# Kernel tuning notes

Hardware: AMD Instinct MI355X
Metric: run time of the kernel (lower is better)

## Reference

```python
import jax, jax.numpy as jnp
import numpy as np
import math

B, S, D = 2, 2048, 2048
H, KV = 16, 4
HD = D // H          # 128
REP = H // KV        # 4


def setup_inputs() -> dict:
    key = jax.random.key(0)
    ks = jax.random.split(key, 6)
    x = jax.random.normal(ks[0], (B, S, D), dtype=jnp.float32)
    wq = jax.random.normal(ks[1], (D, D), dtype=jnp.float32) * (D ** -0.5)
    wk = jax.random.normal(ks[2], (KV * HD, D), dtype=jnp.float32) * (D ** -0.5)
    wv = jax.random.normal(ks[3], (KV * HD, D), dtype=jnp.float32) * (D ** -0.5)
    wo = jax.random.normal(ks[4], (D, D), dtype=jnp.float32) * (D ** -0.5)
    # RoPE frequencies: theta_i = 10000^(-2i/hd), angle = pos * theta_i
    inv_freq = 1.0 / (10000.0 ** (np.arange(0, HD, 2, dtype=np.float32) / HD))
    angles = np.arange(S, dtype=np.float32)[:, None] * inv_freq[None, :]  # [S, HD/2]
    freqs_cos = jnp.asarray(np.cos(angles), dtype=jnp.float32)
    freqs_sin = jnp.asarray(np.sin(angles), dtype=jnp.float32)
    return {"x": x, "wq": wq, "wk": wk, "wv": wv, "wo": wo,
            "freqs_cos": freqs_cos, "freqs_sin": freqs_sin}


def _rope(t, cos, sin):
    # t: [B, S, h, HD]; cos/sin: [S, HD/2]; complex multiply on (even, odd) pairs
    tr = t.reshape(*t.shape[:-1], HD // 2, 2)
    t0, t1 = tr[..., 0], tr[..., 1]
    c = cos[None, :, None, :]
    s = sin[None, :, None, :]
    o0 = t0 * c - t1 * s
    o1 = t0 * s + t1 * c
    return jnp.stack([o0, o1], axis=-1).reshape(t.shape)


def reference(x, wq, wk, wv, wo, freqs_cos, freqs_sin):
    # projections (torch Linear: y = x @ W.T)
    q = jnp.einsum('bsd,ed->bse', x, wq).reshape(B, S, H, HD)
    k = jnp.einsum('bsd,ed->bse', x, wk).reshape(B, S, KV, HD)
    v = jnp.einsum('bsd,ed->bse', x, wv).reshape(B, S, KV, HD)
    q = _rope(q, freqs_cos, freqs_sin)
    k = _rope(k, freqs_cos, freqs_sin)
    # GQA: repeat each kv head REP times -> [B, S, H, HD]
    k = jnp.repeat(k, REP, axis=2)
    v = jnp.repeat(v, REP, axis=2)
    # [B, H, S, HD]
    q = q.transpose(0, 2, 1, 3)
    k = k.transpose(0, 2, 1, 3)
    v = v.transpose(0, 2, 1, 3)
    scores = jnp.einsum('bhqd,bhkd->bhqk', q, k) * (1.0 / math.sqrt(HD))
    # faithful to torch: tril then masked_fill(scores == 0, -inf)
    scores = jnp.tril(scores)
    scores = jnp.where(scores == 0.0, -jnp.inf, scores)
    attn = jax.nn.softmax(scores, axis=-1)
    out = jnp.einsum('bhqk,bhkd->bhqd', attn, v)
    out = out.transpose(0, 2, 1, 3).reshape(B, S, D)
    return jnp.einsum('bsd,ed->bse', out, wo)
```

## Files before the change

kernel.cpp:

```cpp
#include <hip/hip_runtime.h>
#include <stdint.h>

#define B_ 2
#define S_ 2048
#define D_ 2048
#define NH 16
#define NKV 4
#define HD_ 128

typedef unsigned short u16;
typedef unsigned int u32;
typedef __attribute__((ext_vector_type(8))) __bf16 bf16x8;
typedef __attribute__((ext_vector_type(4))) float f32x4;
typedef __attribute__((ext_vector_type(16))) float f32x16;
typedef __attribute__((ext_vector_type(4))) unsigned int u32x4;
typedef __attribute__((ext_vector_type(8))) unsigned short ushort8v;

__device__ __forceinline__ u16 f2bf(float f) {
  u32 u = __builtin_bit_cast(u32, f);
  u32 r = (u + 0x7FFFu + ((u >> 16) & 1u)) >> 16;
  return (u16)r;
}
__device__ __forceinline__ float bf2f(u16 h) {
  return __builtin_bit_cast(float, ((u32)h) << 16);
}
__device__ __forceinline__ u32 cvtpk(float lo, float hi) {
  u32 r;
  asm("v_cvt_pk_bf16_f32 %0, %1, %2" : "=v"(r) : "v"(lo), "v"(hi));
  return r;
}
__device__ __forceinline__ float fexp2(float x) {
  float r;
  asm("v_exp_f32 %0, %1" : "=v"(r) : "v"(x));
  return r;
}
__device__ __forceinline__ f32x16 zero16() {
  f32x16 v;
#pragma unroll
  for (int i = 0; i < 16; ++i) v[i] = 0.f;
  return v;
}

__device__ __forceinline__ void gld_lds16(const void* g, void* l) {
  __builtin_amdgcn_global_load_lds(
      (const __attribute__((address_space(1))) void*)g,
      (__attribute__((address_space(3))) void*)l, 16, 0, 0);
}

#define QSCALE 0.12750527540095196f

__device__ __forceinline__ void cv8(const float* s, u16* d, int i) {
  const float4* sp = (const float4*)s + 2 * (size_t)i;
  float4 a = sp[0], b = sp[1];
  ushort8v o;
  o[0] = f2bf(a.x); o[1] = f2bf(a.y); o[2] = f2bf(a.z); o[3] = f2bf(a.w);
  o[4] = f2bf(b.x); o[5] = f2bf(b.y); o[6] = f2bf(b.z); o[7] = f2bf(b.w);
  *((ushort8v*)d + i) = o;
}
__global__ __launch_bounds__(256) void k_f2b_all(const float* __restrict__ x,
    const float* __restrict__ wq, const float* __restrict__ wk,
    const float* __restrict__ wv, const float* __restrict__ wo,
    u16* __restrict__ xb, u16* __restrict__ wqkv, u16* __restrict__ wob) {
  int i = blockIdx.x * 256 + threadIdx.x;
  if (i < 1048576) { cv8(x, xb, i); return; }
  i -= 1048576;
  if (i < 524288) { cv8(wq, wqkv, i); return; }
  i -= 524288;
  if (i < 131072) { cv8(wk, wqkv + 2048 * 2048, i); return; }
  i -= 131072;
  if (i < 131072) { cv8(wv, wqkv + 2560 * 2048, i); return; }
  i -= 131072;
  if (i < 524288) cv8(wo, wob, i);
}

__global__ __launch_bounds__(256) void k_gemm_qkv(const u16* __restrict__ A,
    const u16* __restrict__ W, u16* __restrict__ Qd, u16* __restrict__ Kd,
    u16* __restrict__ Vd, const float* __restrict__ fc,
    const float* __restrict__ fs, int K) {
  __shared__ char lds[32768];
  char* ldsA = lds;
  char* ldsB = lds + 16384;
  const int tid = threadIdx.x;
  const int lane = tid & 63;
  const int wave = tid >> 6;
  const int m0 = blockIdx.x * 128, n0 = blockIdx.y * 128;
  const int wm = (wave >> 1) * 64, wn = (wave & 1) * 64;
  f32x4 acc[4][4];
#pragma unroll
  for (int i = 0; i < 4; ++i)
#pragma unroll
    for (int j = 0; j < 4; ++j) acc[i][j] = f32x4{0.f, 0.f, 0.f, 0.f};
  const size_t Kb2 = (size_t)K * 2;
  int rowS[4], colS[4];
#pragma unroll
  for (int j = 0; j < 4; ++j) {
    int plin = j * 4096 + tid * 16;
    int o = plin ^ (((plin >> 7) & 7) << 4);
    rowS[j] = o >> 7;
    colS[j] = o & 127;
  }
  for (int kt = 0; kt < K; kt += 64) {
#pragma unroll
    for (int j = 0; j < 4; ++j) {
      gld_lds16((const char*)A + (size_t)(m0 + rowS[j]) * Kb2 + (size_t)kt * 2 + colS[j],
                ldsA + j * 4096 + wave * 1024);
      gld_lds16((const char*)W + (size_t)(n0 + rowS[j]) * Kb2 + (size_t)kt * 2 + colS[j],
                ldsB + j * 4096 + wave * 1024);
    }
    __syncthreads();
#pragma unroll
    for (int kk = 0; kk < 2; ++kk) {
      const int colb = kk * 64 + ((lane >> 4) << 4);
      bf16x8 af[4], bfv[4];
#pragma unroll
      for (int mi = 0; mi < 4; ++mi) {
        int row = wm + mi * 16 + (lane & 15);
        af[mi] = *(const bf16x8*)(ldsA + (row << 7) + (colb ^ ((row & 7) << 4)));
      }
#pragma unroll
      for (int ni = 0; ni < 4; ++ni) {
        int row = wn + ni * 16 + (lane & 15);
        bfv[ni] = *(const bf16x8*)(ldsB + (row << 7) + (colb ^ ((row & 7) << 4)));
      }
#pragma unroll
      for (int mi = 0; mi < 4; ++mi)
#pragma unroll
        for (int ni = 0; ni < 4; ++ni)
          acc[mi][ni] = __builtin_amdgcn_mfma_f32_16x16x32_bf16(af[mi], bfv[ni], acc[mi][ni], 0, 0, 0);
    }
    __syncthreads();
  }
  const int seg = blockIdx.y;
  const int bb = m0 >> 11;
  if (seg < 20) {
    const bool isQ = (seg < 16);
    const int h = isQ ? seg : seg - 16;
    u16* dstB = isQ ? (Qd + ((size_t)(bb * NH + h)) * S_ * HD_)
                    : (Kd + ((size_t)(bb * NKV + h)) * S_ * HD_);
    const float sc = isQ ? QSCALE : 1.0f;
#pragma unroll
    for (int ni = 0; ni < 4; ++ni) {
      const int c = wn + ni * 16 + (lane & 15);
      const int j = c >> 1;
#pragma unroll
      for (int mi = 0; mi < 4; ++mi)
#pragma unroll
        for (int r = 0; r < 4; ++r) {
          const int m = m0 + wm + mi * 16 + ((lane >> 4) << 2) + r;
          const int s = m & 2047;
          float val = acc[mi][ni][r];
          float par = __shfl_xor(val, 1);
          float cs = fc[s * 64 + j], sn = fs[s * 64 + j];
          float outv = (c & 1) ? (par * sn + val * cs) : (val * cs - par * sn);
          dstB[(size_t)s * HD_ + c] = f2bf(outv * sc);
        }
    }
  } else {
    const int h = seg - 20;
    u16* dstB = Vd + ((size_t)(bb * NKV + h)) * S_ * HD_;
#pragma unroll
    for (int ni = 0; ni < 4; ++ni) {
      const int c = wn + ni * 16 + (lane & 15);
#pragma unroll
      for (int mi = 0; mi < 4; ++mi)
#pragma unroll
        for (int r = 0; r < 4; ++r) {
          const int m = m0 + wm + mi * 16 + ((lane >> 4) << 2) + r;
          const int s = m & 2047;
          dstB[(size_t)s * HD_ + c] = f2bf(acc[mi][ni][r]);
        }
    }
  }
}

__global__ __launch_bounds__(512, 1) void k_gemm_out(const u16* __restrict__ A,
    const u16* __restrict__ W, float* __restrict__ C, int N, int K) {
  __shared__ char lds[2][49152];
  const int tid = threadIdx.x, lane = tid & 63, wave = tid >> 6;
  const int wm = wave >> 2, wn = wave & 3;
  const int m0 = blockIdx.x * 256, n0 = blockIdx.y * 128;
  const size_t Kb2 = (size_t)K * 2;
  f32x4 acc[8][2];
#pragma unroll
  for (int mi = 0; mi < 8; ++mi)
#pragma unroll
    for (int ni = 0; ni < 2; ++ni) acc[mi][ni] = f32x4{0.f, 0.f, 0.f, 0.f};
  int rA[4], cA[4], rB[2], cB[2];
#pragma unroll
  for (int j = 0; j < 4; ++j) {
    int p = j * 8192 + tid * 16;
    int o = p ^ (((p >> 7) & 7) << 4);
    rA[j] = o >> 7; cA[j] = o & 127;
  }
#pragma unroll
  for (int j = 0; j < 2; ++j) {
    int p = j * 8192 + tid * 16;
    int o = p ^ (((p >> 7) & 7) << 4);
    rB[j] = o >> 7; cB[j] = o & 127;
  }
  auto stage = [&](int t) {
    char* dst = &lds[t & 1][0];
    const char* As = (const char*)A + (size_t)t * 128;
    const char* Ws = (const char*)W + (size_t)t * 128;
#pragma unroll
    for (int j = 0; j < 4; ++j)
      gld_lds16(As + (size_t)(m0 + rA[j]) * Kb2 + cA[j], dst + j * 8192 + tid * 16);
#pragma unroll
    for (int j = 0; j < 2; ++j)
      gld_lds16(Ws + (size_t)(n0 + rB[j]) * Kb2 + cB[j], dst + 32768 + j * 8192 + tid * 16);
  };
  stage(0);
  __syncthreads();
  const int nt = K >> 6;
  for (int t = 0; t < nt; ++t) {
    if (t + 1 < nt) stage(t + 1);
    const char* buf = &lds[t & 1][0];
#pragma unroll
    for (int kk = 0; kk < 2; ++kk) {
      const int cb = kk * 64 + ((lane >> 4) << 4);
      bf16x8 af[8], bfr[2];
#pragma unroll
      for (int mi = 0; mi < 8; ++mi) {
        int r = wm * 128 + mi * 16 + (lane & 15);
        af[mi] = *(const bf16x8*)(buf + (r << 7) + (cb ^ ((r & 7) << 4)));
      }
#pragma unroll
      for (int ni = 0; ni < 2; ++ni) {
        int r = wn * 32 + ni * 16 + (lane & 15);
        bfr[ni] = *(const bf16x8*)(buf + 32768 + (r << 7) + (cb ^ ((r & 7) << 4)));
      }
      __builtin_amdgcn_s_setprio(1);
#pragma unroll
      for (int mi = 0; mi < 8; ++mi)
#pragma unroll
        for (int ni = 0; ni < 2; ++ni)
          acc[mi][ni] = __builtin_amdgcn_mfma_f32_16x16x32_bf16(af[mi], bfr[ni], acc[mi][ni], 0, 0, 0);
      __builtin_amdgcn_s_setprio(0);
    }
    __syncthreads();
  }
#pragma unroll
  for (int mi = 0; mi < 8; ++mi)
#pragma unroll
    for (int ni = 0; ni < 2; ++ni) {
      const int n = n0 + wn * 32 + ni * 16 + (lane & 15);
#pragma unroll
      for (int r = 0; r < 4; ++r) {
        const int m = m0 + wm * 128 + mi * 16 + ((lane >> 4) << 2) + r;
        C[(size_t)m * N + n] = acc[mi][ni][r];
      }
    }
}

__global__ __launch_bounds__(256, 2) void k_attn(const u16* __restrict__ Q,
    const u16* __restrict__ Kt, const u16* __restrict__ Vt, u16* __restrict__ O) {
  __shared__ char kls[2][16384];
  __shared__ char vls[2][16384];
  const int h = blockIdx.x, b = blockIdx.y;
  const int z = blockIdx.z;
  const int qtb = (z < 8) ? (15 - z) : (z - 8);
  const int tid = threadIdx.x, lane = tid & 63, wave = tid >> 6;
  const int ql = lane & 31, g = lane >> 5;
  const int kvh = h >> 2;
  const u16* Qb = Q + ((size_t)(b * NH + h)) * S_ * HD_;
  const u16* Kb = Kt + ((size_t)(b * NKV + kvh)) * S_ * HD_;
  const u16* Vb = Vt + ((size_t)(b * NKV + kvh)) * S_ * HD_;
  const int q0 = qtb * 128, qw0 = q0 + wave * 32;
  const int qme = qw0 + ql;
  int kRowS[4], kColS[4];
#pragma unroll
  for (int j = 0; j < 4; ++j) {
    int plin = j * 4096 + tid * 16;
    int o = plin ^ (((plin >> 8) & 7) << 4);
    kRowS[j] = o >> 8;
    kColS[j] = o & 255;
  }
  const int kp = tid & 31, hb = (tid >> 5) * 16;
  auto loadV = [&](int tn, u32* vr0, u32* vr1) {
    const u16* vp = Vb + (size_t)(tn * 64 + 2 * kp) * HD_ + hb;
    const u32* r0 = (const u32*)vp;
    const u32* r1 = (const u32*)(vp + HD_);
#pragma unroll
    for (int wd = 0; wd < 8; ++wd) { vr0[wd] = r0[wd]; vr1[wd] = r1[wd]; }
  };
  auto writeV = [&](char* vn, const u32* vr0, const u32* vr1) {
#pragma unroll
    for (int wd = 0; wd < 8; ++wd) {
      u32 v0 = vr0[wd], v1 = vr1[wd];
      u32 lo = (v0 & 0xFFFFu) | (v1 << 16);
      u32 hi = (v0 >> 16) | (v1 & 0xFFFF0000u);
      int hd0 = hb + 2 * wd, hd1 = hd0 + 1;
      *(u32*)(vn + hd0 * 128 + ((4 * kp) ^ ((hd0 & 7) << 4))) = lo;
      *(u32*)(vn + hd1 * 128 + ((4 * kp) ^ ((hd1 & 7) << 4))) = hi;
    }
  };

#pragma unroll
  for (int j = 0; j < 4; ++j)
    gld_lds16((const char*)Kb + (size_t)kRowS[j] * 256 + kColS[j],
              &kls[0][0] + j * 4096 + wave * 1024);
  u32 pv0[8], pv1[8];
  loadV(0, pv0, pv1);
  bf16x8 qf[8];
#pragma unroll
  for (int kk = 0; kk < 8; ++kk)
    qf[kk] = *(const bf16x8*)(Qb + (size_t)qme * HD_ + kk * 16 + g * 8);
  writeV(&vls[0][0], pv0, pv1);
  __syncthreads();

  f32x16 oacc[4];
#pragma unroll
  for (int th = 0; th < 4; ++th) oacc[th] = zero16();
  float mrun = -1e30f, lrun = 0.0f;
  const int nt = 2 * qtb + 2;

  int cur = 0;
  for (int t = 0; t < nt; ++t) {
    const int kv0 = t * 64;
    const bool haveNext = (t + 1 < nt);
    u32 vr0[8], vr1[8];
    if (haveNext) {
      const int kvn = kv0 + 64;
#pragma unroll
      for (int j = 0; j < 4; ++j)
        gld_lds16((const char*)Kb + (size_t)(kvn + kRowS[j]) * 256 + kColS[j],
                  &kls[cur ^ 1][0] + j * 4096 + wave * 1024);
      loadV(t + 1, vr0, vr1);
    }
    if (kv0 <= qw0 + 31) {
      const char* kcur = &kls[cur][0];
      const char* vcur = &vls[cur][0];
      f32x16 c0 = zero16(), c1 = zero16();
      __builtin_amdgcn_s_setprio(1);
#pragma unroll
      for (int kk = 0; kk < 8; ++kk) {
        const int sw = (kk * 32 + 16 * g) ^ ((ql & 7) << 4);
        bf16x8 kf0 = *(const bf16x8*)(kcur + (ql << 8) + sw);
        bf16x8 kf1 = *(const bf16x8*)(kcur + ((32 + ql) << 8) + sw);
        c0 = __builtin_amdgcn_mfma_f32_32x32x16_bf16(kf0, qf[kk], c0, 0, 0, 0);
        c1 = __builtin_amdgcn_mfma_f32_32x32x16_bf16(kf1, qf[kk], c1, 0, 0, 0);
      }
      __builtin_amdgcn_s_setprio(0);
      const bool diag = (kv0 + 63 > qw0);
      float mt = -1e30f;
      if (diag) {
#pragma unroll
        for (int r = 0; r < 16; ++r) {
          float s0 = c0[r], s1 = c1[r];
          int kb = kv0 + (r & 3) + ((r >> 2) << 3) + 4 * g;
          if (kb > qme) s0 = -1e30f;
          if (kb + 32 > qme) s1 = -1e30f;
          c0[r] = s0; c1[r] = s1;
          mt = fmaxf(mt, fmaxf(s0, s1));
        }
      } else {
#pragma unroll
        for (int r = 0; r < 16; ++r)
          mt = fmaxf(mt, fmaxf(c0[r], c1[r]));
      }
      mt = fmaxf(mt, __shfl_xor(mt, 32));
      if (!__all(mt <= mrun + 8.0f)) {
        float mnew = fmaxf(mrun, mt);
        float alpha = fexp2(mrun - mnew);
        lrun *= alpha;
        mrun = mnew;
#pragma unroll
        for (int r = 0; r < 16; ++r) {
          float av = __shfl(alpha, 36 * g + (r & 3) + ((r >> 2) << 3));
          oacc[0][r] *= av; oacc[1][r] *= av;
          oacc[2][r] *= av; oacc[3][r] *= av;
        }
      }
      float lt = 0.0f;
#pragma unroll
      for (int r = 0; r < 16; ++r) {
        float p0 = fexp2(c0[r] - mrun);
        float p1 = fexp2(c1[r] - mrun);
        c0[r] = p0; c1[r] = p1;
        lt += p0 + p1;
      }
      lt += __shfl_xor(lt, 32);
      lrun += lt;
      u32 paw[4][4];
#pragma unroll
      for (int a = 0; a < 2; ++a) {
        {
          u32 X = cvtpk(c0[8 * a + 0], c0[8 * a + 1]);
          u32 Y = cvtpk(c0[8 * a + 2], c0[8 * a + 3]);
          u32 Z = cvtpk(c0[8 * a + 4], c0[8 * a + 5]);
          u32 W = cvtpk(c0[8 * a + 6], c0[8 * a + 7]);
          u32 S1 = g ? X : Z, S2 = g ? Y : W;
          u32 R1 = (u32)__shfl_xor((int)S1, 32), R2 = (u32)__shfl_xor((int)S2, 32);
          paw[a][0] = g ? R1 : X; paw[a][1] = g ? R2 : Y;
          paw[a][2] = g ? Z : R1; paw[a][3] = g ? W : R2;
        }
        {
          u32 X = cvtpk(c1[8 * a + 0], c1[8 * a + 1]);
          u32 Y = cvtpk(c1[8 * a + 2], c1[8 * a + 3]);
          u32 Z = cvtpk(c1[8 * a + 4], c1[8 * a + 5]);
          u32 W = cvtpk(c1[8 * a + 6], c1[8 * a + 7]);
          u32 S1 = g ? X : Z, S2 = g ? Y : W;
          u32 R1 = (u32)__shfl_xor((int)S1, 32), R2 = (u32)__shfl_xor((int)S2, 32);
          paw[2 + a][0] = g ? R1 : X; paw[2 + a][1] = g ? R2 : Y;
          paw[2 + a][2] = g ? Z : R1; paw[2 + a][3] = g ? W : R2;
        }
      }
      __builtin_amdgcn_s_setprio(1);
#pragma unroll
      for (int ks = 0; ks < 4; ++ks) {
        bf16x8 pf = __builtin_bit_cast(bf16x8,
            u32x4{paw[ks][0], paw[ks][1], paw[ks][2], paw[ks][3]});
        const int cb = (32 * ks + 16 * g) ^ ((ql & 7) << 4);
#pragma unroll
        for (int th = 0; th < 4; ++th) {
          bf16x8 vf = *(const bf16x8*)(vcur + ((th * 32 + ql) << 7) + cb);
          oacc[th] = __builtin_amdgcn_mfma_f32_32x32x16_bf16(pf, vf, oacc[th], 0, 0, 0);
        }
      }
      __builtin_amdgcn_s_setprio(0);
    }
    if (haveNext) writeV(&vls[cur ^ 1][0], vr0, vr1);
    __syncthreads();
    cur ^= 1;
  }
#pragma unroll
  for (int r = 0; r < 16; ++r) {
    float lr = __shfl(lrun, 36 * g + (r & 3) + ((r >> 2) << 3));
    float li = 1.0f / lr;
    int q = qw0 + (r & 3) + ((r >> 2) << 3) + 4 * g;
    size_t rowo = (size_t)(b * S_ + q) * D_ + h * HD_ + ql;
#pragma unroll
    for (int th = 0; th < 4; ++th)
      O[rowo + 32 * th] = f2bf(oacc[th][r] * li);
  }
}

extern "C" void kernel_launch(void* const* d_in, const int* in_sizes, int n_in,
                              void* d_out, int out_size, void* d_ws, size_t ws_size,
                              hipStream_t stream) {
  const float* x  = (const float*)d_in[0];
  const float* wq = (const float*)d_in[1];
  const float* wk = (const float*)d_in[2];
  const float* wv = (const float*)d_in[3];
  const float* wo = (const float*)d_in[4];
  const float* fc = (const float*)d_in[5];
  const float* fs = (const float*)d_in[6];
  float* out = (float*)d_out;
  char* ws = (char*)d_ws;
  const size_t MB = 1ull << 20;
  u16* xb   = (u16*)(ws);
  u16* wqkv = (u16*)(ws + 16 * MB);
  u16* wob  = (u16*)(ws + 28 * MB);
  u16* Qb   = (u16*)(ws + 36 * MB);
  u16* Kb   = (u16*)(ws + 52 * MB);
  u16* Vb   = (u16*)(ws + 56 * MB);
  u16* attb = (u16*)(ws);

  k_f2b_all<<<dim3(9216), dim3(256), 0, stream>>>(x, wq, wk, wv, wo, xb, wqkv, wob);

  k_gemm_qkv<<<dim3(32, 24), dim3(256), 0, stream>>>(xb, wqkv, Qb, Kb, Vb, fc, fs, D_);

  k_attn<<<dim3(NH, B_, 16), dim3(256), 0, stream>>>(Qb, Kb, Vb, attb);

  k_gemm_out<<<dim3(16, 16), dim3(512), 0, stream>>>(attb, wob, out, D_, D_);
}
```

Measured before the change: 218.1 us.

## Rewrite QKV GEMM with 256x128 tiles, 8 waves and double-buffered LDS

```diff
diff --git a/kernel.cpp b/kernel.cpp
--- a/kernel.cpp
+++ b/kernel.cpp
@@ -73,60 +73,71 @@
   if (i < 524288) cv8(wo, wob, i);
 }
 
-__global__ __launch_bounds__(256) void k_gemm_qkv(const u16* __restrict__ A,
+__global__ __launch_bounds__(512, 1) void k_gemm_qkv(const u16* __restrict__ A,
     const u16* __restrict__ W, u16* __restrict__ Qd, u16* __restrict__ Kd,
     u16* __restrict__ Vd, const float* __restrict__ fc,
     const float* __restrict__ fs, int K) {
-  __shared__ char lds[32768];
-  char* ldsA = lds;
-  char* ldsB = lds + 16384;
-  const int tid = threadIdx.x;
-  const int lane = tid & 63;
-  const int wave = tid >> 6;
-  const int m0 = blockIdx.x * 128, n0 = blockIdx.y * 128;
-  const int wm = (wave >> 1) * 64, wn = (wave & 1) * 64;
-  f32x4 acc[4][4];
-#pragma unroll
-  for (int i = 0; i < 4; ++i)
-#pragma unroll
-    for (int j = 0; j < 4; ++j) acc[i][j] = f32x4{0.f, 0.f, 0.f, 0.f};
+  __shared__ char lds[2][49152];
+  const int tid = threadIdx.x, lane = tid & 63, wave = tid >> 6;
+  const int wm = wave >> 2, wn = wave & 3;
+  const int m0 = blockIdx.x * 256, n0 = blockIdx.y * 128;
   const size_t Kb2 = (size_t)K * 2;
-  int rowS[4], colS[4];
+  f32x4 acc[8][2];
+#pragma unroll
+  for (int mi = 0; mi < 8; ++mi)
+#pragma unroll
+    for (int ni = 0; ni < 2; ++ni) acc[mi][ni] = f32x4{0.f, 0.f, 0.f, 0.f};
+  int rA[4], cA[4], rB[2], cB[2];
 #pragma unroll
   for (int j = 0; j < 4; ++j) {
-    int plin = j * 4096 + tid * 16;
-    int o = plin ^ (((plin >> 7) & 7) << 4);
-    rowS[j] = o >> 7;
-    colS[j] = o & 127;
-  }
-  for (int kt = 0; kt < K; kt += 64) {
-#pragma unroll
-    for (int j = 0; j < 4; ++j) {
-      gld_lds16((const char*)A + (size_t)(m0 + rowS[j]) * Kb2 + (size_t)kt * 2 + colS[j],
-                ldsA + j * 4096 + wave * 1024);
-      gld_lds16((const char*)W + (size_t)(n0 + rowS[j]) * Kb2 + (size_t)kt * 2 + colS[j],
-                ldsB + j * 4096 + wave * 1024);
-    }
-    __syncthreads();
+    int p = j * 8192 + tid * 16;
+    int o = p ^ (((p >> 7) & 7) << 4);
+    rA[j] = o >> 7; cA[j] = o & 127;
+  }
+#pragma unroll
+  for (int j = 0; j < 2; ++j) {
+    int p = j * 8192 + tid * 16;
+    int o = p ^ (((p >> 7) & 7) << 4);
+    rB[j] = o >> 7; cB[j] = o & 127;
+  }
+  auto stage = [&](int t) {
+    char* dst = &lds[t & 1][0];
+    const char* As = (const char*)A + (size_t)t * 128;
+    const char* Ws = (const char*)W + (size_t)t * 128;
+#pragma unroll
+    for (int j = 0; j < 4; ++j)
+      gld_lds16(As + (size_t)(m0 + rA[j]) * Kb2 + cA[j], dst + j * 8192 + tid * 16);
+#pragma unroll
+    for (int j = 0; j < 2; ++j)
+      gld_lds16(Ws + (size_t)(n0 + rB[j]) * Kb2 + cB[j], dst + 32768 + j * 8192 + tid * 16);
+  };
+  stage(0);
+  __syncthreads();
+  const int nt = K >> 6;
+  for (int t = 0; t < nt; ++t) {
+    if (t + 1 < nt) stage(t + 1);
+    const char* buf = &lds[t & 1][0];
 #pragma unroll
     for (int kk = 0; kk < 2; ++kk) {
-      const int colb = kk * 64 + ((lane >> 4) << 4);
-      bf16x8 af[4], bfv[4];
-#pragma unroll
-      for (int mi = 0; mi < 4; ++mi) {
-        int row = wm + mi * 16 + (lane & 15);
-        af[mi] = *(const bf16x8*)(ldsA + (row << 7) + (colb ^ ((row & 7) << 4)));
-      }
-#pragma unroll
-      for (int ni = 0; ni < 4; ++ni) {
-        int row = wn + ni * 16 + (lane & 15);
-        bfv[ni] = *(const bf16x8*)(ldsB + (row << 7) + (colb ^ ((row & 7) << 4)));
-      }
-#pragma unroll
-      for (int mi = 0; mi < 4; ++mi)
-#pragma unroll
-        for (int ni = 0; ni < 4; ++ni)
-          acc[mi][ni] = __builtin_amdgcn_mfma_f32_16x16x32_bf16(af[mi], bfv[ni], acc[mi][ni], 0, 0, 0);
+      const int cb = kk * 64 + ((lane >> 4) << 4);
+      bf16x8 af[8], bfr[2];
+#pragma unroll
+      for (int mi = 0; mi < 8; ++mi) {
+        int r = wm * 128 + mi * 16 + (lane & 15);
+        af[mi] = *(const bf16x8*)(buf + (r << 7) + (cb ^ ((r & 7) << 4)));
+      }
+#pragma unroll
+      for (int ni = 0; ni < 2; ++ni) {
+        int r = wn * 32 + ni * 16 + (lane & 15);
+        bfr[ni] = *(const bf16x8*)(buf + 32768 + (r << 7) + (cb ^ ((r & 7) << 4)));
+      }
+      __builtin_amdgcn_s_setprio(1);
+#pragma unroll
+      for (int mi = 0; mi < 8; ++mi)
+#pragma unroll
+        for (int ni = 0; ni < 2; ++ni)
+          acc[mi][ni] = __builtin_amdgcn_mfma_f32_16x16x32_bf16(af[mi], bfr[ni], acc[mi][ni], 0, 0, 0);
+      __builtin_amdgcn_s_setprio(0);
     }
     __syncthreads();
   }
@@ -139,14 +150,14 @@
                     : (Kd + ((size_t)(bb * NKV + h)) * S_ * HD_);
     const float sc = isQ ? QSCALE : 1.0f;
 #pragma unroll
-    for (int ni = 0; ni < 4; ++ni) {
-      const int c = wn + ni * 16 + (lane & 15);
+    for (int ni = 0; ni < 2; ++ni) {
+      const int c = (n0 + wn * 32 + ni * 16 + (lane & 15)) & 127;
       const int j = c >> 1;
 #pragma unroll
-      for (int mi = 0; mi < 4; ++mi)
+      for (int mi = 0; mi < 8; ++mi)
 #pragma unroll
         for (int r = 0; r < 4; ++r) {
-          const int m = m0 + wm + mi * 16 + ((lane >> 4) << 2) + r;
+          const int m = m0 + wm * 128 + mi * 16 + ((lane >> 4) << 2) + r;
           const int s = m & 2047;
           float val = acc[mi][ni][r];
           float par = __shfl_xor(val, 1);
@@ -159,13 +170,13 @@
     const int h = seg - 20;
     u16* dstB = Vd + ((size_t)(bb * NKV + h)) * S_ * HD_;
 #pragma unroll
-    for (int ni = 0; ni < 4; ++ni) {
-      const int c = wn + ni * 16 + (lane & 15);
-#pragma unroll
-      for (int mi = 0; mi < 4; ++mi)
+    for (int ni = 0; ni < 2; ++ni) {
+      const int c = (n0 + wn * 32 + ni * 16 + (lane & 15)) & 127;
+#pragma unroll
+      for (int mi = 0; mi < 8; ++mi)
 #pragma unroll
         for (int r = 0; r < 4; ++r) {
-          const int m = m0 + wm + mi * 16 + ((lane >> 4) << 2) + r;
+          const int m = m0 + wm * 128 + mi * 16 + ((lane >> 4) << 2) + r;
           const int s = m & 2047;
           dstB[(size_t)s * HD_ + c] = f2bf(acc[mi][ni][r]);
         }
@@ -458,7 +469,7 @@
 
   k_f2b_all<<<dim3(9216), dim3(256), 0, stream>>>(x, wq, wk, wv, wo, xb, wqkv, wob);
 
-  k_gemm_qkv<<<dim3(32, 24), dim3(256), 0, stream>>>(xb, wqkv, Qb, Kb, Vb, fc, fs, D_);
+  k_gemm_qkv<<<dim3(16, 24), dim3(512), 0, stream>>>(xb, wqkv, Qb, Kb, Vb, fc, fs, D_);
 
   k_attn<<<dim3(NH, B_, 16), dim3(256), 0, stream>>>(Qb, Kb, Vb, attb);
 
```

Measured after the change: 207.9 us. -4.7%, faster.
